# Kernel optimization log

Measured on AMD Instinct MI355X. Metric: run time of the kernel, lower is better.

## Reference

```python
import jax, jax.numpy as jnp
import numpy as np

KS = 3          # deform kernel size
N = KS * KS     # 9 sampling taps per pixel
PAD = 1         # zero padding applied before sampling (nn.ZeroPad2d)
BN_EPS = 1e-5


def conv2d(x, w, b=None, stride=1, padding=0):
    out = jax.lax.conv_general_dilated(
        x, w, (stride, stride), [(padding, padding)] * 2,
        dimension_numbers=('NCHW', 'OIHW', 'NCHW'))
    if b is not None:
        out = out + b[None, :, None, None]
    return out


def setup_inputs() -> dict:
    key = jax.random.key(0)
    ks = jax.random.split(key, 6)
    inC, outC = 128, 256
    B, H, W = 8, 64, 64

    def kaiming(k, shape):
        fan_in = shape[1] * shape[2] * shape[3]
        return jax.random.normal(k, shape, jnp.float32) / np.float32(np.sqrt(fan_in))

    return {
        'x': jax.random.normal(ks[0], (B, inC, H, W), jnp.float32),
        'w_offset': kaiming(ks[1], (2 * N, inC, 3, 3)) * 0.1,  # small offsets, realistic
        'b_offset': jnp.zeros((2 * N,), jnp.float32),
        'w_mask': kaiming(ks[2], (N, inC, 3, 3)),
        'b_mask': jnp.zeros((N,), jnp.float32),
        'w_conv': kaiming(ks[3], (outC, inC, KS, KS)),
        'bn_gamma': jnp.ones((outC,), jnp.float32),
        'bn_beta': jnp.zeros((outC,), jnp.float32),
        'bn_mean': jax.random.normal(ks[4], (outC,), jnp.float32) * 0.1,
        'bn_var': jnp.ones((outC,), jnp.float32) + jax.random.uniform(ks[5], (outC,), jnp.float32) * 0.1,
    }


def deform_conv(x, w_offset, b_offset, w_mask, b_mask, w_conv):
    B, C, H, W = x.shape
    dt = x.dtype

    offset = conv2d(x, w_offset, b_offset, 1, 1)               # (B, 2N, H, W)
    m = jax.nn.sigmoid(conv2d(x, w_mask, b_mask, 1, 1))        # (B, N, H, W)

    # kernel grid offsets p_n (first N channels = rows, last N = cols)
    rng = jnp.arange(-(KS - 1) // 2, (KS - 1) // 2 + 1, dtype=dt)
    pnx, pny = jnp.meshgrid(rng, rng, indexing='ij')
    p_n = jnp.concatenate([pnx.reshape(-1), pny.reshape(-1)])[None, :, None, None]

    # base positions p_0 (torch impl starts at 1, sampling on padded input)
    p0x = jnp.broadcast_to(jnp.arange(1, H + 1, dtype=dt)[:, None], (H, W))
    p0y = jnp.broadcast_to(jnp.arange(1, W + 1, dtype=dt)[None, :], (H, W))
    p_0 = jnp.concatenate([jnp.tile(p0x[None], (N, 1, 1)),
                           jnp.tile(p0y[None], (N, 1, 1))])[None]  # (1, 2N, H, W)

    p = (offset + p_n + p_0).transpose(0, 2, 3, 1)             # (B, H, W, 2N)

    xp = jnp.pad(x, ((0, 0), (0, 0), (PAD, PAD), (PAD, PAD)))
    Hp, Wp = H + 2 * PAD, W + 2 * PAD

    px, py = p[..., :N], p[..., N:]
    fx, fy = jnp.floor(px), jnp.floor(py)
    q_lt_x = jnp.clip(fx, 0, Hp - 1)
    q_lt_y = jnp.clip(fy, 0, Wp - 1)
    q_rb_x = jnp.clip(fx + 1, 0, Hp - 1)
    q_rb_y = jnp.clip(fy + 1, 0, Wp - 1)
    px = jnp.clip(px, 0, Hp - 1)
    py = jnp.clip(py, 0, Wp - 1)

    # bilinear weights (faithful to the reference torch formulas)
    g_lt = (1 + (q_lt_x - px)) * (1 + (q_lt_y - py))
    g_rb = (1 - (q_rb_x - px)) * (1 - (q_rb_y - py))
    g_lb = (1 + (q_lt_x - px)) * (1 - (q_rb_y - py))
    g_rt = (1 - (q_rb_x - px)) * (1 + (q_lt_y - py))

    xp_flat = xp.reshape(B, C, Hp * Wp)

    def gather(qx, qy):
        idx = (qx.astype(jnp.int32) * Wp + qy.astype(jnp.int32)).reshape(B, 1, -1)
        out = jnp.take_along_axis(xp_flat,
                                  jnp.broadcast_to(idx, (B, C, idx.shape[-1])), axis=2)
        return out.reshape(B, C, H, W, N)

    x_off = (g_lt[:, None] * gather(q_lt_x, q_lt_y)
             + g_rb[:, None] * gather(q_rb_x, q_rb_y)
             + g_lb[:, None] * gather(q_lt_x, q_rb_y)
             + g_rt[:, None] * gather(q_rb_x, q_lt_y))       # (B, C, H, W, N)

    x_off = x_off * m.transpose(0, 2, 3, 1)[:, None]          # modulation

    # (B,C,H,W,ks,ks) -> (B,C,H*ks,W*ks)  (equivalent to _reshape_x_offset)
    x_off = x_off.reshape(B, C, H, W, KS, KS).transpose(0, 1, 2, 4, 3, 5)
    x_off = x_off.reshape(B, C, H * KS, W * KS)

    return conv2d(x_off, w_conv, None, KS, 0)                 # (B, outC, H, W)


def reference(x, w_offset, b_offset, w_mask, b_mask, w_conv,
              bn_gamma, bn_beta, bn_mean, bn_var):
    y = deform_conv(x, w_offset, b_offset, w_mask, b_mask, w_conv)
    inv = jax.lax.rsqrt(bn_var + BN_EPS)
    scale = (bn_gamma * inv)[None, :, None, None]
    shift = (bn_beta - bn_mean * bn_gamma * inv)[None, :, None, None]
    return jax.nn.relu(y * scale + shift)
```

## Files before the change

### kernel.cpp

```cpp
#include <hip/hip_runtime.h>
#include <math.h>

#define BB 8
#define CC 128
#define HH 64
#define WW 64
#define NPTS 9
#define OUTC 256
#define HW (HH*WW)
#define KTOT (CC*NPTS)
#define BK 288
#define AP 290
#define WROWS 6

typedef __attribute__((ext_vector_type(8))) short bf16x8;
typedef __attribute__((ext_vector_type(4))) float f32x4;

__device__ unsigned short g_wT[OUTC * KTOT];
__device__ unsigned short g_woT[32 * KTOT];

__device__ __forceinline__ unsigned short f2bf(float f) {
    unsigned int u = __builtin_bit_cast(unsigned int, f);
    unsigned int r = (u + 0x7FFFu + ((u >> 16) & 1u)) >> 16;
    return (unsigned short)r;
}

__device__ __forceinline__ unsigned cvtpk(float lo, float hi) {
    unsigned r;
    asm("v_cvt_pk_bf16_f32 %0, %1, %2" : "=v"(r) : "v"(lo), "v"(hi));
    return r;
}
__device__ __forceinline__ float bflo(unsigned w) { return __builtin_bit_cast(float, w << 16); }
__device__ __forceinline__ float bfhi(unsigned w) { return __builtin_bit_cast(float, w & 0xFFFF0000u); }

__device__ __forceinline__ int orig_k(int k) {
    int cb = k / BK, r = k % BK;
    int pair = r / 18, r2 = r % 18;
    int n = r2 >> 1, half = r2 & 1;
    return (cb * 32 + pair * 2 + half) * NPTS + n;
}

__global__ __launch_bounds__(256) void prep_kernel(
    const float* __restrict__ wo, const float* __restrict__ wm,
    const float* __restrict__ wc)
{
    int idx = blockIdx.x * 256 + threadIdx.x;
    const int T1 = 32 * KTOT;
    if (idx < T1) {
        int nn = idx / KTOT, k = idx - nn * KTOT;
        int ok = orig_k(k);
        float v = (nn < 18) ? wo[nn * KTOT + ok]
                            : (nn < 27 ? wm[(nn - 18) * KTOT + ok] : 0.f);
        g_woT[idx] = f2bf(v);
    } else if (idx < T1 + OUTC * KTOT) {
        int j = idx - T1;
        int oc = j / KTOT, k = j - oc * KTOT;
        g_wT[j] = f2bf(wc[oc * KTOT + orig_k(k)]);
    }
}

struct PF { uint2 w[WROWS]; };

__device__ __forceinline__ void issue(PF& pf, const float* __restrict__ xb,
                                      int h, int g, int tid) {
    if (g >= 8) return;
    int cb = g & 3;
    int q = tid >> 6, col = tid & 63;
    const float* base = xb + (size_t)(cb * 32 + 4 * q) * HW + col;
    #pragma unroll
    for (int r = 0; r < WROWS; ++r) {
        int gr = h - 2 + r;
        bool v = (gr >= 0) & (gr < HH);
        float a0 = v ? base[0 * HW + gr * WW] : 0.f;
        float a1 = v ? base[1 * HW + gr * WW] : 0.f;
        float a2 = v ? base[2 * HW + gr * WW] : 0.f;
        float a3 = v ? base[3 * HW + gr * WW] : 0.f;
        pf.w[r].x = cvtpk(a0, a1);
        pf.w[r].y = cvtpk(a2, a3);
    }
}

__device__ __forceinline__ void commit(uint2* win, const PF& pf, int tid) {
    uint2* wp = win + (tid >> 6) * 384 + (tid & 63);
    #pragma unroll
    for (int r = 0; r < WROWS; ++r) wp[r * 64] = pf.w[r];
}

__global__ __launch_bounds__(512) __attribute__((amdgpu_waves_per_eu(4, 4)))
void fused_kernel(
    const float* __restrict__ x,
    const float* __restrict__ b_offset, const float* __restrict__ b_mask,
    const float* __restrict__ bn_gamma, const float* __restrict__ bn_beta,
    const float* __restrict__ bn_mean,  const float* __restrict__ bn_var,
    float* __restrict__ out)
{
    __shared__ unsigned short Atile[64][AP];
    __shared__ uint2 win[8 * 384];
    __shared__ float params[NPTS][5][64];
    float* ovf = (float*)win;

    int bid = blockIdx.x;
    int blk = (bid & 7) * 64 + (bid >> 3);
    int b = blk >> 6, h = blk & 63;
    int tid  = threadIdx.x;
    int lane = tid & 63;
    int wv   = __builtin_amdgcn_readfirstlane(tid >> 6);
    int l15  = lane & 15;
    int kg   = lane >> 4;
    int spix = lane;

    const float* xb = x + (size_t)b * CC * HW;
    unsigned* AtU = (unsigned*)&Atile[0][0];

    int mi_a = wv & 3, nf_a = wv >> 2;
    f32x4 s1acc = {0.f, 0.f, 0.f, 0.f};

    PF pf; issue(pf, xb, h, 0, tid);
    for (int cb = 0; cb < 4; ++cb) {
        commit(win, pf, tid);
        {
            const uint2* base = win + wv * 384;
            #pragma unroll
            for (int tap = 0; tap < 9; ++tap) {
                int ky = tap / 3, kx = tap % 3;
                int col  = spix + kx - 1;
                int colc = min(max(col, 0), WW - 1);
                uint2 v = base[(ky + 1) * 64 + colc];
                bool cv = (col >= 0) & (col < WW);
                AtU[spix * 145 + (2 * wv) * 9 + tap]     = cv ? v.x : 0u;
                AtU[spix * 145 + (2 * wv + 1) * 9 + tap] = cv ? v.y : 0u;
            }
        }
        issue(pf, xb, h, cb + 1, tid);
        __syncthreads();
        for (int q = 0; q < 9; ++q) {
            int koff = q * 32 + kg * 8;
            bf16x8 af = *(const bf16x8*)&Atile[mi_a * 16 + l15][koff];
            int nn = nf_a * 16 + l15;
            bf16x8 bfr = *(const bf16x8*)&g_woT[nn * KTOT + cb * BK + koff];
            s1acc = __builtin_amdgcn_mfma_f32_16x16x32_bf16(af, bfr, s1acc, 0, 0, 0);
        }
        __syncthreads();
    }

    #pragma unroll
    for (int j = 0; j < 4; ++j) {
        float val = s1acc[j];
        int nn   = nf_a * 16 + l15;
        int pixl = mi_a * 16 + kg * 4 + j;
        if (nn < 9) {
            ovf[nn * 64 + pixl] = val + b_offset[nn] + (float)(nn / 3 - 1) + (float)(h + 1);
        } else if (nn < 18) {
            int n = nn - 9;
            ovf[576 + n * 64 + pixl] = val + b_offset[nn] + (float)(n % 3 - 1) + (float)(pixl + 1);
        } else if (nn < 27) {
            int n = nn - 18;
            float sg = val + b_mask[n];
            ovf[1152 + n * 64 + pixl] = 1.f / (1.f + expf(-sg));
        }
    }
    __syncthreads();

    if (tid < 64) {
        int t = tid;
        #pragma unroll
        for (int n = 0; n < NPTS; ++n) {
            float px = ovf[n * 64 + t];
            float py = ovf[576 + n * 64 + t];
            float m  = ovf[1152 + n * 64 + t];
            float fx = floorf(px), fy = floorf(py);
            float qltx = fminf(fmaxf(fx,       0.f), 65.f);
            float qlty = fminf(fmaxf(fy,       0.f), 65.f);
            float qrbx = fminf(fmaxf(fx + 1.f, 0.f), 65.f);
            float qrby = fminf(fmaxf(fy + 1.f, 0.f), 65.f);
            float pxc  = fminf(fmaxf(px, 0.f), 65.f);
            float pyc  = fminf(fmaxf(py, 0.f), 65.f);
            float glt = (1.f + (qltx - pxc)) * (1.f + (qlty - pyc)) * m;
            float grb = (1.f - (qrbx - pxc)) * (1.f - (qrby - pyc)) * m;
            float glb = (1.f + (qltx - pxc)) * (1.f - (qrby - pyc)) * m;
            float grt = (1.f - (qrbx - pxc)) * (1.f + (qlty - pyc)) * m;
            int i0 = (int)qltx - 1, j0 = (int)qlty - 1;
            int i1 = (int)qrbx - 1, j1 = (int)qrby - 1;
            bool v00 = (i0 >= 0) & (i0 < HH) & (j0 >= 0) & (j0 < WW);
            bool v11 = (i1 >= 0) & (i1 < HH) & (j1 >= 0) & (j1 < WW);
            bool v01 = (i0 >= 0) & (i0 < HH) & (j1 >= 0) & (j1 < WW);
            bool v10 = (i1 >= 0) & (i1 < HH) & (j0 >= 0) & (j0 < WW);
            params[n][0][t] = v00 ? glt : 0.f;
            params[n][1][t] = v11 ? grb : 0.f;
            params[n][2][t] = v01 ? glb : 0.f;
            params[n][3][t] = v10 ? grt : 0.f;
            bool okr0 = ((i0 >= h - 2) & (i0 <= h + 3)) | !(v00 | v01);
            bool okr1 = ((i1 >= h - 2) & (i1 <= h + 3)) | !(v11 | v10);
            bool ok = okr0 & okr1;
            int r0w = min(max(i0 - (h - 2), 0), WROWS - 1);
            int r1w = min(max(i1 - (h - 2), 0), WROWS - 1);
            int r0g = min(max(i0, 0), HH - 1);
            int r1g = min(max(i1, 0), HH - 1);
            int j0c = min(max(j0, 0), WW - 1);
            int j1c = min(max(j1, 0), WW - 1);
            int o  = ok ? (r0w * WW + j0c) : (r0g * WW + j0c);
            int dr = ok ? (r1w - r0w) : (r1g - r0g);
            int dj = j1c - j0c;
            unsigned pk = (unsigned)o | ((unsigned)(dr + 64) << 13)
                        | ((unsigned)(dj + 64) << 20) | ((unsigned)ok << 27);
            params[n][4][t] = __builtin_bit_cast(float, pk);
        }
    }
    __syncthreads();

    f32x4 acc[4][2];
    #pragma unroll
    for (int mi = 0; mi < 4; ++mi)
        #pragma unroll
        for (int ni = 0; ni < 2; ++ni)
            acc[mi][ni] = (f32x4){0.f, 0.f, 0.f, 0.f};

    int oc0 = wv * 32;

    for (int cb = 0; cb < 4; ++cb) {
        commit(win, pf, tid);
        {
            const uint2* baseq = win + wv * 384;
            const float* xg = xb + (size_t)(cb * 32 + 4 * wv) * HW;
            #pragma unroll
            for (int n = 0; n < NPTS; ++n) {
                float g0 = params[n][0][spix];
                float g1 = params[n][1][spix];
                float g2 = params[n][2][spix];
                float g3 = params[n][3][spix];
                unsigned p = __builtin_bit_cast(unsigned, params[n][4][spix]);
                int o  = p & 0x1FFF;
                int d1 = ((int)((p >> 13) & 0x7F) - 64) * WW;
                int d2 = (int)((p >> 20) & 0x7F) - 64;
                float v0, v1, v2, v3;
                if (p & (1u << 27)) {
                    uint2 c00 = baseq[o];
                    uint2 c11 = baseq[o + d1 + d2];
                    uint2 c01 = baseq[o + d2];
                    uint2 c10 = baseq[o + d1];
                    v0 =       g0 * bflo(c00.x);
                    v0 = fmaf(g1, bflo(c11.x), v0);
                    v0 = fmaf(g2, bflo(c01.x), v0);
                    v0 = fmaf(g3, bflo(c10.x), v0);
                    v1 =       g0 * bfhi(c00.x);
                    v1 = fmaf(g1, bfhi(c11.x), v1);
                    v1 = fmaf(g2, bfhi(c01.x), v1);
                    v1 = fmaf(g3, bfhi(c10.x), v1);
                    v2 =       g0 * bflo(c00.y);
                    v2 = fmaf(g1, bflo(c11.y), v2);
                    v2 = fmaf(g2, bflo(c01.y), v2);
                    v2 = fmaf(g3, bflo(c10.y), v2);
                    v3 =       g0 * bfhi(c00.y);
                    v3 = fmaf(g1, bfhi(c11.y), v3);
                    v3 = fmaf(g2, bfhi(c01.y), v3);
                    v3 = fmaf(g3, bfhi(c10.y), v3);
                } else {
                    const float* x0 = xg;
                    const float* x1 = xg + HW;
                    const float* x2 = xg + 2 * HW;
                    const float* x3 = xg + 3 * HW;
                    v0 = g0*x0[o]; v0 = fmaf(g1, x0[o+d1+d2], v0); v0 = fmaf(g2, x0[o+d2], v0); v0 = fmaf(g3, x0[o+d1], v0);
                    v1 = g0*x1[o]; v1 = fmaf(g1, x1[o+d1+d2], v1); v1 = fmaf(g2, x1[o+d2], v1); v1 = fmaf(g3, x1[o+d1], v1);
                    v2 = g0*x2[o]; v2 = fmaf(g1, x2[o+d1+d2], v2); v2 = fmaf(g2, x2[o+d2], v2); v2 = fmaf(g3, x2[o+d1], v2);
                    v3 = g0*x3[o]; v3 = fmaf(g1, x3[o+d1+d2], v3); v3 = fmaf(g2, x3[o+d2], v3); v3 = fmaf(g3, x3[o+d1], v3);
                }
                AtU[spix * 145 + (2 * wv) * 9 + n]     = cvtpk(v0, v1);
                AtU[spix * 145 + (2 * wv + 1) * 9 + n] = cvtpk(v2, v3);
            }
        }
        issue(pf, xb, h, 5 + cb, tid);
        __syncthreads();
        for (int q = 0; q < 9; ++q) {
            int koff = q * 32 + kg * 8;
            bf16x8 af[4];
            #pragma unroll
            for (int mi = 0; mi < 4; ++mi)
                af[mi] = *(const bf16x8*)&Atile[mi * 16 + l15][koff];
            #pragma unroll
            for (int ni = 0; ni < 2; ++ni) {
                int oc = oc0 + ni * 16 + l15;
                bf16x8 bfr = *(const bf16x8*)&g_wT[oc * KTOT + cb * BK + koff];
                #pragma unroll
                for (int mi = 0; mi < 4; ++mi)
                    acc[mi][ni] = __builtin_amdgcn_mfma_f32_16x16x32_bf16(af[mi], bfr, acc[mi][ni], 0, 0, 0);
            }
        }
        __syncthreads();
    }

    #pragma unroll
    for (int ni = 0; ni < 2; ++ni) {
        int oc = oc0 + ni * 16 + l15;
        float inv   = 1.f / sqrtf(bn_var[oc] + 1e-5f);
        float scale = bn_gamma[oc] * inv;
        float shift = bn_beta[oc] - bn_mean[oc] * scale;
        float* op = out + ((size_t)b * OUTC + oc) * HW + h * WW + kg * 4;
        #pragma unroll
        for (int mi = 0; mi < 4; ++mi) {
            f32x4 o4;
            #pragma unroll
            for (int j = 0; j < 4; ++j) {
                float v = fmaf(acc[mi][ni][j], scale, shift);
                o4[j] = v > 0.f ? v : 0.f;
            }
            *(f32x4*)(op + mi * 16) = o4;
        }
    }
}

extern "C" void kernel_launch(void* const* d_in, const int* in_sizes, int n_in,
                              void* d_out, int out_size, void* d_ws, size_t ws_size,
                              hipStream_t stream) {
    (void)in_sizes; (void)n_in; (void)out_size; (void)d_ws; (void)ws_size;
    const float* x        = (const float*)d_in[0];
    const float* w_offset = (const float*)d_in[1];
    const float* b_offset = (const float*)d_in[2];
    const float* w_mask   = (const float*)d_in[3];
    const float* b_mask   = (const float*)d_in[4];
    const float* w_conv   = (const float*)d_in[5];
    const float* bn_gamma = (const float*)d_in[6];
    const float* bn_beta  = (const float*)d_in[7];
    const float* bn_mean  = (const float*)d_in[8];
    const float* bn_var   = (const float*)d_in[9];
    float* out = (float*)d_out;

    int prep_elems = 32 * KTOT + OUTC * KTOT;
    prep_kernel<<<(prep_elems + 255) / 256, 256, 0, stream>>>(w_offset, w_mask, w_conv);
    fused_kernel<<<BB * HH, 512, 0, stream>>>(x, b_offset, b_mask,
                                              bn_gamma, bn_beta, bn_mean, bn_var, out);
}
```

Measured before the change: 85.33 us.

## Double block to 1024 threads, splitting taps and output channels across wave halves

Launches 16 waves per block instead of 8. The two wave halves split the 9 sampling taps (0-3 vs 4-8) during im2col and bilinear gathering, and each wave now owns 16 output channels instead of 32 in the main MFMA GEMM. Only the first 8 waves run the offset/mask GEMM. The aim is more latency hiding and fewer registers per wave at waves_per_eu 8, at the cost of duplicated A-tile LDS reads, redundant global prefetch by both halves, and uneven tap splitting.

```diff
diff --git a/kernel.cpp b/kernel.cpp
--- a/kernel.cpp
+++ b/kernel.cpp
@@ -62,11 +62,11 @@
 struct PF { uint2 w[WROWS]; };
 
 __device__ __forceinline__ void issue(PF& pf, const float* __restrict__ xb,
-                                      int h, int g, int tid) {
+                                      int h, int g, int wv, int lane) {
     if (g >= 8) return;
     int cb = g & 3;
-    int q = tid >> 6, col = tid & 63;
-    const float* base = xb + (size_t)(cb * 32 + 4 * q) * HW + col;
+    int q = wv & 7;
+    const float* base = xb + (size_t)(cb * 32 + 4 * q) * HW + lane;
     #pragma unroll
     for (int r = 0; r < WROWS; ++r) {
         int gr = h - 2 + r;
@@ -80,13 +80,13 @@
     }
 }
 
-__device__ __forceinline__ void commit(uint2* win, const PF& pf, int tid) {
-    uint2* wp = win + (tid >> 6) * 384 + (tid & 63);
+__device__ __forceinline__ void commit(uint2* win, const PF& pf, int wv, int lane) {
+    uint2* wp = win + (wv & 7) * 384 + lane;
     #pragma unroll
     for (int r = 0; r < WROWS; ++r) wp[r * 64] = pf.w[r];
 }
 
-__global__ __launch_bounds__(512) __attribute__((amdgpu_waves_per_eu(4, 4)))
+__global__ __launch_bounds__(1024) __attribute__((amdgpu_waves_per_eu(8, 8)))
 void fused_kernel(
     const float* __restrict__ x,
     const float* __restrict__ b_offset, const float* __restrict__ b_mask,
@@ -112,51 +112,71 @@
     const float* xb = x + (size_t)b * CC * HW;
     unsigned* AtU = (unsigned*)&Atile[0][0];
 
-    int mi_a = wv & 3, nf_a = wv >> 2;
+    int q8 = wv & 7;
+    int th = wv >> 3;
+
+    int mi_a = wv & 3, nf_a = (wv >> 2) & 1;
     f32x4 s1acc = {0.f, 0.f, 0.f, 0.f};
 
-    PF pf; issue(pf, xb, h, 0, tid);
+    PF pf; issue(pf, xb, h, 0, wv, lane);
     for (int cb = 0; cb < 4; ++cb) {
-        commit(win, pf, tid);
+        commit(win, pf, wv, lane);
         {
-            const uint2* base = win + wv * 384;
-            #pragma unroll
-            for (int tap = 0; tap < 9; ++tap) {
-                int ky = tap / 3, kx = tap % 3;
-                int col  = spix + kx - 1;
-                int colc = min(max(col, 0), WW - 1);
-                uint2 v = base[(ky + 1) * 64 + colc];
-                bool cv = (col >= 0) & (col < WW);
-                AtU[spix * 145 + (2 * wv) * 9 + tap]     = cv ? v.x : 0u;
-                AtU[spix * 145 + (2 * wv + 1) * 9 + tap] = cv ? v.y : 0u;
-            }
-        }
-        issue(pf, xb, h, cb + 1, tid);
+            const uint2* base = win + q8 * 384;
+            if (th == 0) {
+                #pragma unroll
+                for (int tap = 0; tap < 4; ++tap) {
+                    int ky = tap / 3, kx = tap % 3;
+                    int col  = spix + kx - 1;
+                    int colc = min(max(col, 0), WW - 1);
+                    uint2 v = base[(ky + 1) * 64 + colc];
+                    bool cv = (col >= 0) & (col < WW);
+                    AtU[spix * 145 + (2 * q8) * 9 + tap]     = cv ? v.x : 0u;
+                    AtU[spix * 145 + (2 * q8 + 1) * 9 + tap] = cv ? v.y : 0u;
+                }
+            } else {
+                #pragma unroll
+                for (int tap = 4; tap < 9; ++tap) {
+                    int ky = tap / 3, kx = tap % 3;
+                    int col  = spix + kx - 1;
+                    int colc = min(max(col, 0), WW - 1);
+                    uint2 v = base[(ky + 1) * 64 + colc];
+                    bool cv = (col >= 0) & (col < WW);
+                    AtU[spix * 145 + (2 * q8) * 9 + tap]     = cv ? v.x : 0u;
+                    AtU[spix * 145 + (2 * q8 + 1) * 9 + tap] = cv ? v.y : 0u;
+                }
+            }
+        }
+        issue(pf, xb, h, cb + 1, wv, lane);
         __syncthreads();
-        for (int q = 0; q < 9; ++q) {
-            int koff = q * 32 + kg * 8;
-            bf16x8 af = *(const bf16x8*)&Atile[mi_a * 16 + l15][koff];
-            int nn = nf_a * 16 + l15;
-            bf16x8 bfr = *(const bf16x8*)&g_woT[nn * KTOT + cb * BK + koff];
-            s1acc = __builtin_amdgcn_mfma_f32_16x16x32_bf16(af, bfr, s1acc, 0, 0, 0);
+        if (wv < 8) {
+            for (int q = 0; q < 9; ++q) {
+                int koff = q * 32 + kg * 8;
+                bf16x8 af = *(const bf16x8*)&Atile[mi_a * 16 + l15][koff];
+                int nn = nf_a * 16 + l15;
+                bf16x8 bfr = *(const bf16x8*)&g_woT[nn * KTOT + cb * BK + koff];
+                s1acc = __builtin_amdgcn_mfma_f32_16x16x32_bf16(af, bfr, s1acc, 0, 0, 0);
+            }
         }
         __syncthreads();
     }
 
-    #pragma unroll
-    for (int j = 0; j < 4; ++j) {
-        float val = s1acc[j];
-        int nn   = nf_a * 16 + l15;
-        int pixl = mi_a * 16 + kg * 4 + j;
-        if (nn < 9) {
-            ovf[nn * 64 + pixl] = val + b_offset[nn] + (float)(nn / 3 - 1) + (float)(h + 1);
-        } else if (nn < 18) {
-            int n = nn - 9;
-            ovf[576 + n * 64 + pixl] = val + b_offset[nn] + (float)(n % 3 - 1) + (float)(pixl + 1);
-        } else if (nn < 27) {
-            int n = nn - 18;
-            float sg = val + b_mask[n];
-            ovf[1152 + n * 64 + pixl] = 1.f / (1.f + expf(-sg));
+    if (wv < 8) {
+        #pragma unroll
+        for (int j = 0; j < 4; ++j) {
+            float val = s1acc[j];
+            int nn   = nf_a * 16 + l15;
+            int pixl = mi_a * 16 + kg * 4 + j;
+            if (nn < 9) {
+                ovf[nn * 64 + pixl] = val + b_offset[nn] + (float)(nn / 3 - 1) + (float)(h + 1);
+            } else if (nn < 18) {
+                int n = nn - 9;
+                ovf[576 + n * 64 + pixl] = val + b_offset[nn] + (float)(n % 3 - 1) + (float)(pixl + 1);
+            } else if (nn < 27) {
+                int n = nn - 18;
+                float sg = val + b_mask[n];
+                ovf[1152 + n * 64 + pixl] = 1.f / (1.f + expf(-sg));
+            }
         }
     }
     __syncthreads();
@@ -208,22 +228,20 @@
     }
     __syncthreads();
 
-    f32x4 acc[4][2];
+    f32x4 acc[4];
     #pragma unroll
-    for (int mi = 0; mi < 4; ++mi)
-        #pragma unroll
-        for (int ni = 0; ni < 2; ++ni)
-            acc[mi][ni] = (f32x4){0.f, 0.f, 0.f, 0.f};
-
-    int oc0 = wv * 32;
+    for (int mi = 0; mi < 4; ++mi) acc[mi] = (f32x4){0.f, 0.f, 0.f, 0.f};
+
+    int oc0 = wv * 16;
 
     for (int cb = 0; cb < 4; ++cb) {
-        commit(win, pf, tid);
+        commit(win, pf, wv, lane);
         {
-            const uint2* baseq = win + wv * 384;
-            const float* xg = xb + (size_t)(cb * 32 + 4 * wv) * HW;
-            #pragma unroll
-            for (int n = 0; n < NPTS; ++n) {
+            const uint2* baseq = win + q8 * 384;
+            const float* xg = xb + (size_t)(cb * 32 + 4 * q8) * HW;
+            int n0 = th ? 4 : 0, n1 = th ? 9 : 4;
+            #pragma unroll 5
+            for (int n = n0; n < n1; ++n) {
                 float g0 = params[n][0][spix];
                 float g1 = params[n][1][spix];
                 float g2 = params[n][2][spix];
@@ -264,11 +282,11 @@
                     v2 = g0*x2[o]; v2 = fmaf(g1, x2[o+d1+d2], v2); v2 = fmaf(g2, x2[o+d2], v2); v2 = fmaf(g3, x2[o+d1], v2);
                     v3 = g0*x3[o]; v3 = fmaf(g1, x3[o+d1+d2], v3); v3 = fmaf(g2, x3[o+d2], v3); v3 = fmaf(g3, x3[o+d1], v3);
                 }
-                AtU[spix * 145 + (2 * wv) * 9 + n]     = cvtpk(v0, v1);
-                AtU[spix * 145 + (2 * wv + 1) * 9 + n] = cvtpk(v2, v3);
-            }
-        }
-        issue(pf, xb, h, 5 + cb, tid);
+                AtU[spix * 145 + (2 * q8) * 9 + n]     = cvtpk(v0, v1);
+                AtU[spix * 145 + (2 * q8 + 1) * 9 + n] = cvtpk(v2, v3);
+            }
+        }
+        issue(pf, xb, h, 5 + cb, wv, lane);
         __syncthreads();
         for (int q = 0; q < 9; ++q) {
             int koff = q * 32 + kg * 8;
@@ -276,21 +294,17 @@
             #pragma unroll
             for (int mi = 0; mi < 4; ++mi)
                 af[mi] = *(const bf16x8*)&Atile[mi * 16 + l15][koff];
+            int oc = oc0 + l15;
+            bf16x8 bfr = *(const bf16x8*)&g_wT[oc * KTOT + cb * BK + koff];
             #pragma unroll
-            for (int ni = 0; ni < 2; ++ni) {
-                int oc = oc0 + ni * 16 + l15;
-                bf16x8 bfr = *(const bf16x8*)&g_wT[oc * KTOT + cb * BK + koff];
-                #pragma unroll
-                for (int mi = 0; mi < 4; ++mi)
-                    acc[mi][ni] = __builtin_amdgcn_mfma_f32_16x16x32_bf16(af[mi], bfr, acc[mi][ni], 0, 0, 0);
-            }
+            for (int mi = 0; mi < 4; ++mi)
+                acc[mi] = __builtin_amdgcn_mfma_f32_16x16x32_bf16(af[mi], bfr, acc[mi], 0, 0, 0);
         }
         __syncthreads();
     }
 
-    #pragma unroll
-    for (int ni = 0; ni < 2; ++ni) {
-        int oc = oc0 + ni * 16 + l15;
+    {
+        int oc = oc0 + l15;
         float inv   = 1.f / sqrtf(bn_var[oc] + 1e-5f);
         float scale = bn_gamma[oc] * inv;
         float shift = bn_beta[oc] - bn_mean[oc] * scale;
@@ -300,7 +314,7 @@
             f32x4 o4;
             #pragma unroll
             for (int j = 0; j < 4; ++j) {
-                float v = fmaf(acc[mi][ni][j], scale, shift);
+                float v = fmaf(acc[mi][j], scale, shift);
                 o4[j] = v > 0.f ? v : 0.f;
             }
             *(f32x4*)(op + mi * 16) = o4;
@@ -326,6 +340,6 @@
 
     int prep_elems = 32 * KTOT + OUTC * KTOT;
     prep_kernel<<<(prep_elems + 255) / 256, 256, 0, stream>>>(w_offset, w_mask, w_conv);
-    fused_kernel<<<BB * HH, 512, 0, stream>>>(x, b_offset, b_mask,
-                                              bn_gamma, bn_beta, bn_mean, bn_var, out);
-}
+    fused_kernel<<<BB * HH, 1024, 0, stream>>>(x, b_offset, b_mask,
+                                               bn_gamma, bn_beta, bn_mean, bn_var, out);
+}
```

New measurement: 98.16 us. 1.15x slower.
